# Optimization experiments

Measured on AMD Instinct MI355X. Metric: run time of the kernel, lower is better.

The kernel has to match this reference:

```python
import jax, jax.numpy as jnp
import numpy as np

EMBED_DIM = 256
NUM_CLASSES = 10


def setup_inputs() -> dict:
    key = jax.random.key(0)
    k1, k2, k3, k4 = jax.random.split(key, 4)
    x = jax.random.normal(k1, (64, 196, 768), dtype=jnp.float32)
    ag_w = jax.random.normal(k2, (EMBED_DIM, 768), dtype=jnp.float32)
    ag_b = jax.random.normal(k3, (EMBED_DIM,), dtype=jnp.float32)
    lm_w = jax.random.normal(k4, (EMBED_DIM * NUM_CLASSES, 768), dtype=jnp.float32)
    return {"x": x, "ag_w": ag_w, "ag_b": ag_b, "lm_w": lm_w}


def reference(x, ag_w, ag_b, lm_w):
    # x: (B, HW, D); ag_w: (E, D); ag_b: (E,); lm_w: (E*C, D)
    B, HW, D = x.shape
    E, C = EMBED_DIM, NUM_CLASSES
    # frozen arrangement generator -> binary sign pattern (B, HW, E)
    sign_patterns = (jnp.einsum('bhd,ed->bhe', x, ag_w) + ag_b > 0).astype(x.dtype)
    # linear map: (B, HW, E*C) -> (B, HW, E, C)
    z = jnp.einsum('bhd,pd->bhp', x, lm_w).reshape(B, HW, E, C)
    # masked reduction over HW and embed dims
    preds = jnp.einsum('bhp,bhpc->bc', sign_patterns, z) / HW
    return preds / E
```

## Files before the change

### kernel.cpp

```cpp
#include <hip/hip_runtime.h>

#define B_    64
#define HW_   196
#define HWP_  224
#define D_    768
#define E_    256
#define C_    10
#define MP_   (B_*HWP_)
#define K3K_  (E_*D_)
#define K3NB_ 256

typedef __bf16 bf16x8 __attribute__((ext_vector_type(8)));
typedef __bf16 bf16x4 __attribute__((ext_vector_type(4)));
typedef __bf16 bf16x2 __attribute__((ext_vector_type(2)));
typedef float  f32x4  __attribute__((ext_vector_type(4)));

__device__ __forceinline__ void gld_lds16(const void* g, void* l) {
  __builtin_amdgcn_global_load_lds((const __attribute__((address_space(1))) void*)g,
                                   (__attribute__((address_space(3))) void*)l, 16, 0, 0);
}

__global__ __launch_bounds__(256) void k0_prep(const float* __restrict__ w,
                                               __bf16* __restrict__ whi,
                                               __bf16* __restrict__ wlo) {
  size_t i4 = ((size_t)blockIdx.x * 256 + threadIdx.x) * 4;
  float4 v = *(const float4*)&w[i4];
  float vv[4] = {v.x, v.y, v.z, v.w};
  bf16x4 h, l;
#pragma unroll
  for (int j = 0; j < 4; j++) {
    __bf16 hj = (__bf16)vv[j];
    float r = vv[j] - (float)hj;
    h[j] = hj;
    l[j] = (__bf16)r;
  }
  *(bf16x4*)&whi[i4] = h;
  *(bf16x4*)&wlo[i4] = l;
}

__global__ __launch_bounds__(256) void k1_signs(const float* __restrict__ x,
                                                const __bf16* __restrict__ whi,
                                                const __bf16* __restrict__ wlo,
                                                const float* __restrict__ bias,
                                                __bf16* __restrict__ st) {
  __shared__ __align__(16) char smem[118784];
  const int m0 = blockIdx.x * 64;
  const int tid = threadIdx.x;
  const int wave = tid >> 6, lane = tid & 63;
  const int wn = wave * 64;
  const int q = lane >> 4, l15 = lane & 15;
  const int swq = (q ^ ((l15 >> 1) & 3)) * 8;

  const int ar = tid >> 2, ac = (tid & 3) * 8;
  const int am = m0 + ar;
  const int ab = am / HWP_;
  const int ahp = am - ab * HWP_;
  const bool avalid = (ahp < HW_);
  const float* aptr = &x[((size_t)ab * HW_ + (avalid ? ahp : 0)) * D_ + ac];

  const int swB = ((tid & 3) ^ ((tid >> 3) & 3)) * 8;
  const size_t offB = (size_t)(tid >> 2) * D_ + swB;

  f32x4 acc[4][4] = {};
  float4 aX0, aX1, aY0, aY1;

#define K1_LOADA(r0, r1, kk) do { \
    r0 = *(const float4*)&aptr[(kk)]; \
    r1 = *(const float4*)&aptr[(kk) + 4]; \
  } while (0)

#define K1_CONV(bufA, r0, r1) do { \
    __bf16* AhW = (__bf16*)(smem + 98304 + (bufA) * 10240); \
    __bf16* AlW = AhW + 2560; \
    float va[8] = {r0.x, r0.y, r0.z, r0.w, r1.x, r1.y, r1.z, r1.w}; \
    bf16x8 hh, ll; \
    _Pragma("unroll") \
    for (int j = 0; j < 8; j++) { \
      float vj = avalid ? va[j] : 0.0f; \
      __bf16 hj = (__bf16)vj; float rr = vj - (float)hj; \
      hh[j] = hj; ll[j] = (__bf16)rr; \
    } \
    *(bf16x8*)&AhW[ar * 40 + ac] = hh; \
    *(bf16x8*)&AlW[ar * 40 + ac] = ll; \
  } while (0)

#define K1_DMAB(buf3, kk) do { \
    char* bb = smem + (buf3) * 32768; \
    _Pragma("unroll") \
    for (int c = 0; c < 4; c++) { \
      gld_lds16(&whi[offB + (size_t)c * 64 * D_ + (kk)], bb + c * 4096 + wave * 1024); \
      gld_lds16(&wlo[offB + (size_t)c * 64 * D_ + (kk)], bb + 16384 + c * 4096 + wave * 1024); \
    } \
  } while (0)

#define K1_COMPUTE(buf3, bufA) do { \
    const __bf16* BhL = (const __bf16*)(smem + (buf3) * 32768); \
    const __bf16* BlL = BhL + 8192; \
    const __bf16* AhL = (const __bf16*)(smem + 98304 + (bufA) * 10240); \
    const __bf16* AlL = AhL + 2560; \
    bf16x8 ah[4], al[4], bh[4], bl[4]; \
    _Pragma("unroll") \
    for (int t = 0; t < 4; t++) { \
      int ra = (t * 16 + l15) * 40 + q * 8; \
      int rb = (wn + t * 16 + l15) * 32 + swq; \
      ah[t] = *(const bf16x8*)&AhL[ra]; \
      al[t] = *(const bf16x8*)&AlL[ra]; \
      bh[t] = *(const bf16x8*)&BhL[rb]; \
      bl[t] = *(const bf16x8*)&BlL[rb]; \
    } \
    __builtin_amdgcn_s_setprio(1); \
    _Pragma("unroll") \
    for (int mt = 0; mt < 4; mt++) \
      _Pragma("unroll") \
      for (int nt = 0; nt < 4; nt++) { \
        acc[mt][nt] = __builtin_amdgcn_mfma_f32_16x16x32_bf16(ah[mt], bh[nt], acc[mt][nt], 0, 0, 0); \
        acc[mt][nt] = __builtin_amdgcn_mfma_f32_16x16x32_bf16(al[mt], bh[nt], acc[mt][nt], 0, 0, 0); \
        acc[mt][nt] = __builtin_amdgcn_mfma_f32_16x16x32_bf16(ah[mt], bl[nt], acc[mt][nt], 0, 0, 0); \
      } \
    __builtin_amdgcn_s_setprio(0); \
  } while (0)

#define K1_BAR() do { \
    asm volatile("s_waitcnt lgkmcnt(0)" ::: "memory"); \
    __builtin_amdgcn_s_barrier(); \
    __builtin_amdgcn_sched_barrier(0); \
  } while (0)

  K1_DMAB(0, 0);
  __builtin_amdgcn_sched_barrier(0);
  K1_LOADA(aX0, aX1, 0);
  __builtin_amdgcn_sched_barrier(0);
  K1_DMAB(1, 32);
  __builtin_amdgcn_sched_barrier(0);
  K1_LOADA(aY0, aY1, 32);
  K1_CONV(0, aX0, aX1);
  K1_BAR();

#pragma unroll
  for (int t = 0; t < 22; ++t) {
    K1_DMAB((t + 2) % 3, (t + 2) * 32);
    __builtin_amdgcn_sched_barrier(0);
    if ((t & 1) == 0) K1_LOADA(aX0, aX1, (t + 2) * 32);
    else              K1_LOADA(aY0, aY1, (t + 2) * 32);
    K1_COMPUTE(t % 3, t & 1);
    if ((t & 1) == 0) K1_CONV(1, aY0, aY1);
    else              K1_CONV(0, aX0, aX1);
    K1_BAR();
  }
  K1_COMPUTE(22 % 3, 0);
  K1_CONV(1, aY0, aY1);
  K1_BAR();
  K1_COMPUTE(23 % 3, 1);
  K1_BAR();

#undef K1_LOADA
#undef K1_CONV
#undef K1_DMAB
#undef K1_COMPUTE
#undef K1_BAR

  __bf16* Sload = (__bf16*)smem;
#pragma unroll
  for (int mt = 0; mt < 4; mt++)
#pragma unroll
    for (int nt = 0; nt < 4; nt++) {
      int e = wn + nt * 16 + l15;
      float bv = bias[e];
      bf16x4 o;
#pragma unroll
      for (int r = 0; r < 4; r++) {
        int m = m0 + mt * 16 + q * 4 + r;
        int b = m / HWP_;
        int hp = m - b * HWP_;
        float v = acc[mt][nt][r] + bv;
        o[r] = (hp < HW_ && v > 0.0f) ? (__bf16)1.0f : (__bf16)0.0f;
      }
      *(bf16x4*)&Sload[e * 72 + mt * 16 + q * 4] = o;
    }
  __syncthreads();
#pragma unroll
  for (int it = 0; it < 16; it++) {
    int e = (tid >> 4) + it * 16;
    int m4 = (tid & 15) * 4;
    bf16x4 v = *(const bf16x4*)&Sload[e * 72 + m4];
    int mabs = m0 + m4;
    int b = mabs / HWP_;
    int hp = mabs - b * HWP_;
    *(bf16x4*)&st[((size_t)b * E_ + e) * HWP_ + hp] = v;
  }
}

__global__ __launch_bounds__(512) void k2_g(const __bf16* __restrict__ st,
                                            const float* __restrict__ x,
                                            __bf16* __restrict__ g) {
  __shared__ __align__(16) __bf16 As[2][256 * 32];
  __shared__ __align__(16) __bf16 Bs[2][128 * 40];
  const int f = blockIdx.x;
  const int xcd = f & 7;
  const int slot = f >> 3;
  const int b  = xcd + 8 * (slot / 6);
  const int d0 = (slot % 6) * 128;
  const int tid = threadIdx.x;
  const int wave = tid >> 6, lane = tid & 63;
  const int WE = (wave & 3) * 64;
  const int WD = (wave >> 2) * 64;
  const int q = lane >> 4, l15 = lane & 15;
  const int ar = tid >> 2, ac = (tid & 3) * 8;
  const int ldA = wave * 512;
  const int dg = tid & 31, kp = tid >> 5;
  f32x4 acc[4][4] = {};

  const __bf16* gA = &st[((size_t)b * E_ + ar) * HWP_ + ac];
  const float4 zero4 = make_float4(0.f, 0.f, 0.f, 0.f);
  float4 f0, f1;

#define K2_STAGEA(buf, kk) do { \
    gld_lds16(gA + (kk),                       &As[buf][ldA]); \
    gld_lds16(gA + (size_t)128 * HWP_ + (kk),  &As[buf][4096 + ldA]); \
  } while (0)

#define K2_LOADB(kk) do { \
    int hp0 = (kk) + 2 * kp; \
    const float* bsrc = &x[((size_t)b * HW_ + hp0) * D_ + d0 + 4 * dg]; \
    f0 = (hp0     < HW_) ? *(const float4*)&bsrc[0]  : zero4; \
    f1 = (hp0 + 1 < HW_) ? *(const float4*)&bsrc[D_] : zero4; \
  } while (0)

#define K2_WRITEB(buf) do { \
    float rr0[4] = {f0.x, f0.y, f0.z, f0.w}; \
    float rr1[4] = {f1.x, f1.y, f1.z, f1.w}; \
    _Pragma("unroll") \
    for (int j = 0; j < 4; j++) { \
      bf16x2 o; \
      o[0] = (__bf16)rr0[j]; o[1] = (__bf16)rr1[j]; \
      *(bf16x2*)&Bs[buf][(4 * dg + j) * 40 + 2 * kp] = o; \
    } \
  } while (0)

  K2_STAGEA(0, 0);
  K2_LOADB(0);
  K2_WRITEB(0);
  __syncthreads();

  int cur = 0;
  for (int k0 = 0; k0 < HWP_; k0 += 32) {
    const bool have = (k0 + 32 < HWP_);
    if (have) {
      K2_STAGEA(cur ^ 1, k0 + 32);
      K2_LOADB(k0 + 32);
    }
    bf16x8 af[4], bfr[4];
#pragma unroll
    for (int t = 0; t < 4; t++) {
      af[t]  = *(const bf16x8*)&As[cur][(WE + t * 16 + l15) * 32 + q * 8];
      bfr[t] = *(const bf16x8*)&Bs[cur][(WD + t * 16 + l15) * 40 + q * 8];
    }
#pragma unroll
    for (int mt = 0; mt < 4; mt++)
#pragma unroll
      for (int nt = 0; nt < 4; nt++)
        acc[mt][nt] = __builtin_amdgcn_mfma_f32_16x16x32_bf16(af[mt], bfr[nt], acc[mt][nt], 0, 0, 0);
    if (have) K2_WRITEB(cur ^ 1);
    __syncthreads();
    cur ^= 1;
  }
#undef K2_STAGEA
#undef K2_LOADB
#undef K2_WRITEB

#pragma unroll
  for (int mt = 0; mt < 4; mt++)
#pragma unroll
    for (int nt = 0; nt < 4; nt++) {
      int d = d0 + WD + nt * 16 + l15;
#pragma unroll
      for (int r = 0; r < 4; r++) {
        int e = WE + mt * 16 + q * 4 + r;
        g[((size_t)b * E_ + e) * D_ + d] = (__bf16)acc[mt][nt][r];
      }
    }
}

__global__ __launch_bounds__(256) void k3_mfma(const __bf16* __restrict__ g,
                                               const float* __restrict__ lmw,
                                               float* __restrict__ part) {
  __shared__ float sp[B_ * C_];
  const int tid = threadIdx.x;
  const int wave = tid >> 6, lane = tid & 63;
  const int q = lane >> 4, l15 = lane & 15;
  const int e = blockIdx.x;
  f32x4 acc[4] = {};

  for (int i = tid; i < B_ * C_; i += 256) sp[i] = 0.0f;

#pragma unroll
  for (int ks = 0; ks < 6; ks++) {
    int d = wave * 192 + ks * 32 + q * 8;
    size_t k = (size_t)e * D_ + d;
    bf16x8 bfrag;
    if (l15 < C_) {
      const float* bp = &lmw[((size_t)e * C_ + l15) * D_ + d];
      float4 b0 = *(const float4*)&bp[0];
      float4 b1 = *(const float4*)&bp[4];
      float bb[8] = {b0.x, b0.y, b0.z, b0.w, b1.x, b1.y, b1.z, b1.w};
#pragma unroll
      for (int j = 0; j < 8; j++) bfrag[j] = (__bf16)bb[j];
    } else {
#pragma unroll
      for (int j = 0; j < 8; j++) bfrag[j] = (__bf16)0.0f;
    }
#pragma unroll
    for (int mt = 0; mt < 4; mt++) {
      bf16x8 afrag = *(const bf16x8*)&g[(size_t)(mt * 16 + l15) * K3K_ + k];
      acc[mt] = __builtin_amdgcn_mfma_f32_16x16x32_bf16(afrag, bfrag, acc[mt], 0, 0, 0);
    }
  }
  __syncthreads();
  if (l15 < C_) {
#pragma unroll
    for (int mt = 0; mt < 4; mt++)
#pragma unroll
      for (int r = 0; r < 4; r++) {
        int b = mt * 16 + q * 4 + r;
        atomicAdd(&sp[b * C_ + l15], acc[mt][r]);
      }
  }
  __syncthreads();
  for (int i = tid; i < B_ * C_; i += 256)
    part[(size_t)blockIdx.x * (B_ * C_) + i] = sp[i];
}

__global__ __launch_bounds__(256) void k4_reduce(const float* __restrict__ part,
                                                 float* __restrict__ out) {
  __shared__ float sp[256];
  const int b = blockIdx.x;
  const int tid = threadIdx.x;
  const int c = tid & 15, g16 = tid >> 4;
  float s = 0.0f;
  if (c < C_) {
#pragma unroll
    for (int j = 0; j < 16; j++)
      s += part[(size_t)(g16 + 16 * j) * (B_ * C_) + b * C_ + c];
  }
  sp[tid] = s;
  __syncthreads();
  if (tid < C_) {
    float t = 0.0f;
#pragma unroll
    for (int j = 0; j < 16; j++) t += sp[j * 16 + tid];
    out[b * C_ + tid] = t * (1.0f / (196.0f * 256.0f));
  }
}

extern "C" void kernel_launch(void* const* d_in, const int* in_sizes, int n_in,
                              void* d_out, int out_size, void* d_ws, size_t ws_size,
                              hipStream_t stream) {
  const float* x    = (const float*)d_in[0];
  const float* ag_w = (const float*)d_in[1];
  const float* ag_b = (const float*)d_in[2];
  const float* lm_w = (const float*)d_in[3];
  float* out = (float*)d_out;

  char* ws = (char*)d_ws;
  const size_t W_BYTES  = (size_t)E_ * D_ * 2;
  const size_t ST_BYTES = (size_t)B_ * E_ * HWP_ * 2;
  const size_t G_BYTES  = (size_t)B_ * E_ * D_ * 2;
  __bf16* whi  = (__bf16*)(ws);
  __bf16* wlo  = (__bf16*)(ws + W_BYTES);
  __bf16* st   = (__bf16*)(ws + 2 * W_BYTES);
  __bf16* gb   = (__bf16*)(ws + 2 * W_BYTES + ST_BYTES);
  float*  part = (float*)(ws + 2 * W_BYTES + ST_BYTES + G_BYTES);

  k0_prep<<<dim3(192), dim3(256), 0, stream>>>(ag_w, whi, wlo);
  k1_signs<<<dim3(MP_ / 64), dim3(256), 0, stream>>>(x, whi, wlo, ag_b, st);
  k2_g<<<dim3(6 * B_), dim3(512), 0, stream>>>(st, x, gb);
  k3_mfma<<<dim3(K3NB_), dim3(256), 0, stream>>>(gb, lm_w, part);
  k4_reduce<<<dim3(B_), dim3(256), 0, stream>>>(part, out);
}
```

Before: 148.1 us.

## Fuse lm_w contraction into G GEMM epilogue and drop intermediate G buffer

The G GEMM kernel no longer writes the bf16 G tensor to global memory. Each block stages its G tile in shared memory, contracts it against the matching lm_w slice with scalar FP32 FMAs, and reduces the result to per-block class partials. A tiny single-block kernel then sums these partials. This removes the large G write/read round trip and a launch, at the cost of each block re-reading lm_w slices, mostly from L2, and extra shared-memory syncs in the epilogue.

```diff
diff --git a/kernel.cpp b/kernel.cpp
--- a/kernel.cpp
+++ b/kernel.cpp
@@ -7,8 +7,6 @@
 #define E_    256
 #define C_    10
 #define MP_   (B_*HWP_)
-#define K3K_  (E_*D_)
-#define K3NB_ 256
 
 typedef __bf16 bf16x8 __attribute__((ext_vector_type(8)));
 typedef __bf16 bf16x4 __attribute__((ext_vector_type(4)));
@@ -190,11 +188,13 @@
   }
 }
 
-__global__ __launch_bounds__(512) void k2_g(const __bf16* __restrict__ st,
-                                            const float* __restrict__ x,
-                                            __bf16* __restrict__ g) {
-  __shared__ __align__(16) __bf16 As[2][256 * 32];
-  __shared__ __align__(16) __bf16 Bs[2][128 * 40];
+__global__ __launch_bounds__(512) void k2_fused(const __bf16* __restrict__ st,
+                                                const float* __restrict__ x,
+                                                const float* __restrict__ lmw,
+                                                float* __restrict__ part) {
+  __shared__ __align__(16) char smem2[53248];
+  __bf16* As = (__bf16*)smem2;
+  __bf16* Bs = (__bf16*)(smem2 + 32768);
   const int f = blockIdx.x;
   const int xcd = f & 7;
   const int slot = f >> 3;
@@ -215,8 +215,8 @@
   float4 f0, f1;
 
 #define K2_STAGEA(buf, kk) do { \
-    gld_lds16(gA + (kk),                       &As[buf][ldA]); \
-    gld_lds16(gA + (size_t)128 * HWP_ + (kk),  &As[buf][4096 + ldA]); \
+    gld_lds16(gA + (kk),                       &As[(buf) * 8192 + ldA]); \
+    gld_lds16(gA + (size_t)128 * HWP_ + (kk),  &As[(buf) * 8192 + 4096 + ldA]); \
   } while (0)
 
 #define K2_LOADB(kk) do { \
@@ -233,7 +233,7 @@
     for (int j = 0; j < 4; j++) { \
       bf16x2 o; \
       o[0] = (__bf16)rr0[j]; o[1] = (__bf16)rr1[j]; \
-      *(bf16x2*)&Bs[buf][(4 * dg + j) * 40 + 2 * kp] = o; \
+      *(bf16x2*)&Bs[(buf) * 5120 + (4 * dg + j) * 40 + 2 * kp] = o; \
     } \
   } while (0)
 
@@ -252,8 +252,8 @@
     bf16x8 af[4], bfr[4];
 #pragma unroll
     for (int t = 0; t < 4; t++) {
-      af[t]  = *(const bf16x8*)&As[cur][(WE + t * 16 + l15) * 32 + q * 8];
-      bfr[t] = *(const bf16x8*)&Bs[cur][(WD + t * 16 + l15) * 40 + q * 8];
+      af[t]  = *(const bf16x8*)&As[cur * 8192 + (WE + t * 16 + l15) * 32 + q * 8];
+      bfr[t] = *(const bf16x8*)&Bs[cur * 5120 + (WD + t * 16 + l15) * 40 + q * 8];
     }
 #pragma unroll
     for (int mt = 0; mt < 4; mt++)
@@ -268,87 +268,83 @@
 #undef K2_LOADB
 #undef K2_WRITEB
 
-#pragma unroll
-  for (int mt = 0; mt < 4; mt++)
-#pragma unroll
-    for (int nt = 0; nt < 4; nt++) {
-      int d = d0 + WD + nt * 16 + l15;
-#pragma unroll
-      for (int r = 0; r < 4; r++) {
-        int e = WE + mt * 16 + q * 4 + r;
-        g[((size_t)b * E_ + e) * D_ + d] = (__bf16)acc[mt][nt][r];
+  __bf16* Gl = (__bf16*)smem2;
+  float pc[10];
+#pragma unroll
+  for (int c = 0; c < 10; c++) pc[c] = 0.0f;
+  const int eh = WE & 127;
+  const int myhalf = WE >> 7;
+  const int er = tid >> 2;
+  const int seg = tid & 3;
+
+  for (int p = 0; p < 2; p++) {
+    if (myhalf == p) {
+#pragma unroll
+      for (int mt = 0; mt < 4; mt++)
+#pragma unroll
+        for (int nt = 0; nt < 4; nt++) {
+          int row = eh + mt * 16 + q * 4;
+          int col = WD + nt * 16 + l15;
+#pragma unroll
+          for (int r = 0; r < 4; r++)
+            Gl[(row + r) * 136 + col] = (__bf16)acc[mt][nt][r];
+        }
+    }
+    __syncthreads();
+    {
+      bf16x8 gv[4];
+#pragma unroll
+      for (int j = 0; j < 4; j++)
+        gv[j] = *(const bf16x8*)&Gl[er * 136 + seg * 32 + j * 8];
+      float gf[32];
+#pragma unroll
+      for (int j = 0; j < 32; j++) gf[j] = (float)gv[j >> 3][j & 7];
+      int eglob = p * 128 + er;
+#pragma unroll
+      for (int c = 0; c < 10; c++) {
+        const float* wp = &lmw[((size_t)eglob * C_ + c) * D_ + d0 + seg * 32];
+        float s = 0.0f;
+#pragma unroll
+        for (int j4 = 0; j4 < 8; j4++) {
+          float4 w4 = *(const float4*)&wp[j4 * 4];
+          s += gf[j4 * 4 + 0] * w4.x + gf[j4 * 4 + 1] * w4.y +
+               gf[j4 * 4 + 2] * w4.z + gf[j4 * 4 + 3] * w4.w;
+        }
+        pc[c] += s;
       }
     }
-}
-
-__global__ __launch_bounds__(256) void k3_mfma(const __bf16* __restrict__ g,
-                                               const float* __restrict__ lmw,
-                                               float* __restrict__ part) {
-  __shared__ float sp[B_ * C_];
-  const int tid = threadIdx.x;
-  const int wave = tid >> 6, lane = tid & 63;
-  const int q = lane >> 4, l15 = lane & 15;
-  const int e = blockIdx.x;
-  f32x4 acc[4] = {};
-
-  for (int i = tid; i < B_ * C_; i += 256) sp[i] = 0.0f;
-
-#pragma unroll
-  for (int ks = 0; ks < 6; ks++) {
-    int d = wave * 192 + ks * 32 + q * 8;
-    size_t k = (size_t)e * D_ + d;
-    bf16x8 bfrag;
-    if (l15 < C_) {
-      const float* bp = &lmw[((size_t)e * C_ + l15) * D_ + d];
-      float4 b0 = *(const float4*)&bp[0];
-      float4 b1 = *(const float4*)&bp[4];
-      float bb[8] = {b0.x, b0.y, b0.z, b0.w, b1.x, b1.y, b1.z, b1.w};
-#pragma unroll
-      for (int j = 0; j < 8; j++) bfrag[j] = (__bf16)bb[j];
-    } else {
-#pragma unroll
-      for (int j = 0; j < 8; j++) bfrag[j] = (__bf16)0.0f;
-    }
-#pragma unroll
-    for (int mt = 0; mt < 4; mt++) {
-      bf16x8 afrag = *(const bf16x8*)&g[(size_t)(mt * 16 + l15) * K3K_ + k];
-      acc[mt] = __builtin_amdgcn_mfma_f32_16x16x32_bf16(afrag, bfrag, acc[mt], 0, 0, 0);
-    }
+    __syncthreads();
+  }
+#pragma unroll
+  for (int c = 0; c < 10; c++)
+#pragma unroll
+    for (int off = 32; off >= 1; off >>= 1)
+      pc[c] += __shfl_xor(pc[c], off, 64);
+  float* sp = (float*)smem2;
+  if (lane == 0) {
+#pragma unroll
+    for (int c = 0; c < 10; c++) sp[wave * 10 + c] = pc[c];
   }
   __syncthreads();
-  if (l15 < C_) {
-#pragma unroll
-    for (int mt = 0; mt < 4; mt++)
-#pragma unroll
-      for (int r = 0; r < 4; r++) {
-        int b = mt * 16 + q * 4 + r;
-        atomicAdd(&sp[b * C_ + l15], acc[mt][r]);
-      }
-  }
-  __syncthreads();
-  for (int i = tid; i < B_ * C_; i += 256)
-    part[(size_t)blockIdx.x * (B_ * C_) + i] = sp[i];
-}
-
-__global__ __launch_bounds__(256) void k4_reduce(const float* __restrict__ part,
-                                                 float* __restrict__ out) {
-  __shared__ float sp[256];
-  const int b = blockIdx.x;
-  const int tid = threadIdx.x;
-  const int c = tid & 15, g16 = tid >> 4;
-  float s = 0.0f;
-  if (c < C_) {
-#pragma unroll
-    for (int j = 0; j < 16; j++)
-      s += part[(size_t)(g16 + 16 * j) * (B_ * C_) + b * C_ + c];
-  }
-  sp[tid] = s;
-  __syncthreads();
-  if (tid < C_) {
-    float t = 0.0f;
-#pragma unroll
-    for (int j = 0; j < 16; j++) t += sp[j * 16 + tid];
-    out[b * C_ + tid] = t * (1.0f / (196.0f * 256.0f));
+  if (tid < 10) {
+    float s = 0.0f;
+#pragma unroll
+    for (int w = 0; w < 8; w++) s += sp[w * 10 + tid];
+    part[(size_t)f * 10 + tid] = s;
+  }
+}
+
+__global__ __launch_bounds__(640) void k4_final(const float* __restrict__ part,
+                                                float* __restrict__ out) {
+  int t = threadIdx.x;
+  if (t < B_ * C_) {
+    int b = t / C_, c = t - b * C_;
+    int xcd = b & 7, bhi = b >> 3;
+    float s = 0.0f;
+#pragma unroll
+    for (int j = 0; j < 6; j++)
+      s += part[(size_t)(xcd + 8 * (bhi * 6 + j)) * C_ + c];
+    out[t] = s * (1.0f / (196.0f * 256.0f));
   }
 }
 
@@ -364,16 +360,13 @@
   char* ws = (char*)d_ws;
   const size_t W_BYTES  = (size_t)E_ * D_ * 2;
   const size_t ST_BYTES = (size_t)B_ * E_ * HWP_ * 2;
-  const size_t G_BYTES  = (size_t)B_ * E_ * D_ * 2;
   __bf16* whi  = (__bf16*)(ws);
   __bf16* wlo  = (__bf16*)(ws + W_BYTES);
   __bf16* st   = (__bf16*)(ws + 2 * W_BYTES);
-  __bf16* gb   = (__bf16*)(ws + 2 * W_BYTES + ST_BYTES);
-  float*  part = (float*)(ws + 2 * W_BYTES + ST_BYTES + G_BYTES);
+  float*  part = (float*)(ws + 2 * W_BYTES + ST_BYTES);
 
   k0_prep<<<dim3(192), dim3(256), 0, stream>>>(ag_w, whi, wlo);
   k1_signs<<<dim3(MP_ / 64), dim3(256), 0, stream>>>(x, whi, wlo, ag_b, st);
-  k2_g<<<dim3(6 * B_), dim3(512), 0, stream>>>(st, x, gb);
-  k3_mfma<<<dim3(K3NB_), dim3(256), 0, stream>>>(gb, lm_w, part);
-  k4_reduce<<<dim3(B_), dim3(256), 0, stream>>>(part, out);
-}
+  k2_fused<<<dim3(6 * B_), dim3(512), 0, stream>>>(st, x, lm_w, part);
+  k4_final<<<dim3(1), dim3(640), 0, stream>>>(part, out);
+}
```

Result: slower. 272.4 us (+83.9%).
